# Optimization experiments

Measured on AMD Instinct MI355X. Metric: run time of the kernel, lower is better.

Reference implementation:

```python
import jax, jax.numpy as jnp
import numpy as np


def setup_inputs() -> dict:
    key = jax.random.key(0)
    k1, k2, k3 = jax.random.split(key, 3)
    B, H, S, D = 2, 8, 4096, 64
    queries = jax.random.normal(k1, (B, H, S, D), dtype=jnp.float32)
    keys = jax.random.normal(k2, (B, H, S, D), dtype=jnp.float32)
    values = jax.random.normal(k3, (B, H, S, D), dtype=jnp.float32)
    mask = jnp.zeros((1, 1, S, S), dtype=jnp.float32)
    return {"queries": queries, "keys": keys, "values": values, "d_k": D, "mask": mask}


def reference(queries, keys, values, d_k, mask):
    # scores: [B, H, Sq, Sk]
    scale = 1.0 / jnp.sqrt(jnp.asarray(d_k, dtype=queries.dtype))
    scores = jnp.einsum("bhqd,bhkd->bhqk", queries, keys) * scale
    scores = scores + (-1e9) * mask  # additive mask, broadcasts over B, H
    weights = jax.nn.softmax(scores, axis=-1)
    return jnp.einsum("bhqk,bhkd->bhqd", weights, values)
```

## Files before the change

kernel.cpp:

```cpp
#include <hip/hip_runtime.h>

#define S_LEN 4096
#define DHEAD 64
#define BQ    128
#define BK    64
#define NT    (S_LEN / BK)
#define KPAD  72
#define NBH   16
#define TILE_HALFS (BK * DHEAD)
#define WS_KV_HALFS ((size_t)NBH * NT * TILE_HALFS)

typedef __fp16   pk16x2 __attribute__((ext_vector_type(2)));
typedef _Float16 half4v __attribute__((ext_vector_type(4)));
typedef _Float16 half8  __attribute__((ext_vector_type(8)));
typedef float    f32x4  __attribute__((ext_vector_type(4)));

__device__ __forceinline__ void gl_lds16(const _Float16* g, _Float16* l) {
    __builtin_amdgcn_global_load_lds(
        (const __attribute__((address_space(1))) unsigned int*)g,
        (__attribute__((address_space(3))) unsigned int*)l, 16, 0, 0);
}

__global__ void mask_flag_kernel(const float4* __restrict__ mask, int* __restrict__ flag) {
    const long stride = 2048L * 256;
    long i = (long)blockIdx.x * 256 + threadIdx.x;
    int nz = 0;
    #pragma unroll
    for (int it = 0; it < 8; ++it) {
        float4 a = mask[i + it * stride];
        nz |= (a.x != 0.f) | (a.y != 0.f) | (a.z != 0.f) | (a.w != 0.f);
    }
    if (__any(nz)) {
        if ((threadIdx.x & 63) == 0) atomicOr(flag, 1);
    }
}

__global__ void conv_kernel(const float* __restrict__ Kg, const float* __restrict__ Vg,
                            const float* __restrict__ mask,
                            _Float16* __restrict__ wsK, _Float16* __restrict__ wsV,
                            int* __restrict__ flag) {
    const int tid  = threadIdx.x;
    const int tile = blockIdx.x;
    __shared__ __align__(16) _Float16 T[64][64];

    if (blockIdx.y == 0) {
        const float* Ksrc = Kg + (long)tile * TILE_HALFS;
        _Float16*    dst  = wsK + (long)tile * TILE_HALFS;
        #pragma unroll
        for (int it = 0; it < 2; ++it) {
            int m = tid + it * 256;
            int r = m >> 3, c = m & 7;
            const float4* s4 = (const float4*)(Ksrc + r * DHEAD + ((c ^ (r & 7)) << 3));
            float4 a = s4[0], b = s4[1];
            union { pk16x2 p[4]; half8 h; } u;
            u.p[0] = __builtin_amdgcn_cvt_pkrtz(a.x, a.y);
            u.p[1] = __builtin_amdgcn_cvt_pkrtz(a.z, a.w);
            u.p[2] = __builtin_amdgcn_cvt_pkrtz(b.x, b.y);
            u.p[3] = __builtin_amdgcn_cvt_pkrtz(b.z, b.w);
            *(half8*)(dst + m * 8) = u.h;
        }
    } else if (blockIdx.y == 1) {
        const float* Vsrc = Vg + (long)tile * TILE_HALFS;
        const int r  = tid >> 2;
        const int d0 = (tid & 3) << 4;
        const float4* s4 = (const float4*)(Vsrc + r * DHEAD + d0);
        float vv[16];
        *(float4*)&vv[0]  = s4[0];
        *(float4*)&vv[4]  = s4[1];
        *(float4*)&vv[8]  = s4[2];
        *(float4*)&vv[12] = s4[3];
        #pragma unroll
        for (int j = 0; j < 16; j += 2) {
            pk16x2 p = __builtin_amdgcn_cvt_pkrtz(vv[j], vv[j + 1]);
            T[d0 + j][r]     = *((_Float16*)&p);
            T[d0 + j + 1][r] = *((_Float16*)&p + 1);
        }
        __syncthreads();
        _Float16* dst = wsV + (long)tile * TILE_HALFS;
        #pragma unroll
        for (int it = 0; it < 2; ++it) {
            int m = tid + it * 256;
            int d = m >> 3, c = m & 7;
            *(half8*)(dst + m * 8) = *(const half8*)&T[d][(c ^ (d & 7)) << 3];
        }
    } else {
        const float4* m4 = (const float4*)mask;
        const long stride = 1024L * 256;
        long i = (long)blockIdx.x * 256 + tid;
        int nz = 0;
        #pragma unroll
        for (int it = 0; it < 16; ++it) {
            float4 a = m4[i + it * stride];
            nz |= (a.x != 0.f) | (a.y != 0.f) | (a.z != 0.f) | (a.w != 0.f);
        }
        if (__any(nz)) {
            if ((tid & 63) == 0) atomicOr(flag, 1);
        }
    }
}

__global__ __launch_bounds__(256, 4) void attn_ws_kernel(
    const float* __restrict__ Q, const _Float16* __restrict__ KW,
    const _Float16* __restrict__ VW, const int* __restrict__ dk,
    const float* __restrict__ mask, const int* __restrict__ maskflag,
    float* __restrict__ O)
{
    const int qt   = blockIdx.x;
    const int bh   = blockIdx.y;
    const int tid  = threadIdx.x;
    const int wave = tid >> 6;
    const int lane = tid & 63;
    const int l15  = lane & 15;
    const int quad = lane >> 4;
    const int sw   = (l15 & 7) << 3;
    const int rq8  = quad << 3;

    const long base = (long)bh * S_LEN * DHEAD;
    const float* Qh = Q + base;
    float*       Oh = O + base;
    const _Float16* gk = KW + (long)bh * (NT * TILE_HALFS);
    const _Float16* gv = VW + (long)bh * (NT * TILE_HALFS);

    const int q0 = qt * 64 + wave * 16;
    const float csq  = rsqrtf((float)dk[0]) * 1.44269504088896f;
    const float mfac = -1e9f * 1.44269504088896f;
    const bool use_mask = (maskflag[0] != 0);

    __shared__ __align__(16) _Float16 KT[2][TILE_HALFS];
    __shared__ __align__(16) _Float16 VT[2][TILE_HALFS];
    __shared__ __align__(16) _Float16 Pw[4][16][64];

    half8 qf[2];
    #pragma unroll
    for (int kc = 0; kc < 2; ++kc) {
        const float4* src = (const float4*)(Qh + (long)(q0 + l15) * DHEAD + kc*32 + rq8);
        float4 a = src[0], b = src[1];
        union { pk16x2 p[4]; half8 h; } u;
        u.p[0] = __builtin_amdgcn_cvt_pkrtz(a.x*csq, a.y*csq);
        u.p[1] = __builtin_amdgcn_cvt_pkrtz(a.z*csq, a.w*csq);
        u.p[2] = __builtin_amdgcn_cvt_pkrtz(b.x*csq, b.y*csq);
        u.p[3] = __builtin_amdgcn_cvt_pkrtz(b.z*csq, b.w*csq);
        qf[kc] = u.h;
    }

    auto stage = [&](int kt, int b) {
        const _Float16* k8 = gk + (long)kt * TILE_HALFS + tid * 8;
        const _Float16* v8 = gv + (long)kt * TILE_HALFS + tid * 8;
        gl_lds16(k8,        &KT[b][tid * 8]);
        gl_lds16(k8 + 2048, &KT[b][2048 + tid * 8]);
        gl_lds16(v8,        &VT[b][tid * 8]);
        gl_lds16(v8 + 2048, &VT[b][2048 + tid * 8]);
    };

    f32x4 o[4];
    #pragma unroll
    for (int dt = 0; dt < 4; ++dt) o[dt] = (f32x4){0.f, 0.f, 0.f, 0.f};
    float m_i = -INFINITY;
    float l_i = 0.0f;

    stage(0, 0);
    __syncthreads();

    for (int kt = 0; kt < NT; ++kt) {
        const int b = kt & 1;
        if (kt + 1 < NT) stage(kt + 1, b ^ 1);

        f32x4 st[4];
        #pragma unroll
        for (int nt = 0; nt < 4; ++nt) st[nt] = (f32x4){0.f,0.f,0.f,0.f};
        __builtin_amdgcn_s_setprio(1);
        #pragma unroll
        for (int nt = 0; nt < 4; ++nt) {
            const int rb = (nt << 10) + (l15 << 6);
            #pragma unroll
            for (int kc = 0; kc < 2; ++kc) {
                half8 af = *(const half8*)&KT[b][rb + ((kc*32 + rq8) ^ sw)];
                st[nt] = __builtin_amdgcn_mfma_f32_16x16x32_f16(af, qf[kc], st[nt], 0, 0, 0);
            }
        }
        __builtin_amdgcn_s_setprio(0);

        if (use_mask) {
            const long mrow = (long)(q0 + l15) * S_LEN + kt*BK;
            #pragma unroll
            for (int nt = 0; nt < 4; ++nt)
                #pragma unroll
                for (int r = 0; r < 4; ++r)
                    st[nt][r] += mfac * mask[mrow + nt*16 + quad*4 + r];
        }

        {
            float mx = fmaxf(fmaxf(fmaxf(st[0][0], st[0][1]), fmaxf(st[0][2], st[0][3])),
                             fmaxf(fmaxf(st[1][0], st[1][1]), fmaxf(st[1][2], st[1][3])));
            float mx2 = fmaxf(fmaxf(fmaxf(st[2][0], st[2][1]), fmaxf(st[2][2], st[2][3])),
                              fmaxf(fmaxf(st[3][0], st[3][1]), fmaxf(st[3][2], st[3][3])));
            mx = fmaxf(mx, mx2);
            mx = fmaxf(mx, __shfl_xor(mx, 16, 64));
            mx = fmaxf(mx, __shfl_xor(mx, 32, 64));
            const bool need = __any(mx > m_i);
            const float mnew = need ? fmaxf(m_i, mx) : m_i;
            float rsum = 0.0f;
            #pragma unroll
            for (int nt = 0; nt < 4; ++nt) {
                #pragma unroll
                for (int r = 0; r < 4; ++r) {
                    float p = __builtin_amdgcn_exp2f(st[nt][r] - mnew);
                    st[nt][r] = p;
                    rsum += p;
                }
            }
            rsum += __shfl_xor(rsum, 16, 64);
            rsum += __shfl_xor(rsum, 32, 64);
            if (need) {
                const float alpha = __builtin_amdgcn_exp2f(m_i - mnew);
                #pragma unroll
                for (int r = 0; r < 4; ++r) {
                    float a_r = __shfl(alpha, quad*4 + r, 64);
                    #pragma unroll
                    for (int dt = 0; dt < 4; ++dt) o[dt][r] *= a_r;
                }
                l_i = alpha * l_i + rsum;
                m_i = mnew;
            } else {
                l_i += rsum;
            }
        }

        #pragma unroll
        for (int nt = 0; nt < 4; ++nt) {
            union { pk16x2 p[2]; half4v h; } up;
            up.p[0] = __builtin_amdgcn_cvt_pkrtz(st[nt][0], st[nt][1]);
            up.p[1] = __builtin_amdgcn_cvt_pkrtz(st[nt][2], st[nt][3]);
            *(half4v*)&Pw[wave][l15][(nt*16 + quad*4) ^ sw] = up.h;
        }

        __builtin_amdgcn_s_setprio(1);
        #pragma unroll
        for (int kc2 = 0; kc2 < 2; ++kc2) {
            half8 pa = *(const half8*)&Pw[wave][l15][(kc2*32 + rq8) ^ sw];
            #pragma unroll
            for (int dt = 0; dt < 4; ++dt) {
                const int db = (dt << 10) + (l15 << 6);
                half8 vb = *(const half8*)&VT[b][db + ((kc2*32 + rq8) ^ sw)];
                o[dt] = __builtin_amdgcn_mfma_f32_16x16x32_f16(pa, vb, o[dt], 0, 0, 0);
            }
        }
        __builtin_amdgcn_s_setprio(0);

        if (kt + 1 < NT) __syncthreads();
    }

    #pragma unroll
    for (int r = 0; r < 4; ++r) {
        float lq = __shfl(l_i, quad*4 + r, 64);
        float linv = __builtin_amdgcn_rcpf(lq);
        const long row = (long)(q0 + quad*4 + r) * DHEAD;
        #pragma unroll
        for (int dt = 0; dt < 4; ++dt)
            Oh[row + dt*16 + l15] = o[dt][r] * linv;
    }
}

__global__ __launch_bounds__(256, 2) void attn_kernel_fb(
    const float* __restrict__ Q, const float* __restrict__ K,
    const float* __restrict__ V, const int* __restrict__ dk,
    const float* __restrict__ mask, const int* __restrict__ maskflag,
    float* __restrict__ O)
{
    const int qt   = blockIdx.x;
    const int bh   = blockIdx.y;
    const int tid  = threadIdx.x;
    const int wave = tid >> 6;
    const int lane = tid & 63;
    const int l15  = lane & 15;
    const int quad = lane >> 4;

    const long base = (long)bh * S_LEN * DHEAD;
    const float* Qh = Q + base;
    const float* Kh = K + base;
    const float* Vh = V + base;
    float*       Oh = O + base;

    const int q0 = qt * BQ + wave * 32;
    const float csq  = rsqrtf((float)dk[0]) * 1.44269504088896f;
    const float mfac = -1e9f * 1.44269504088896f;
    const bool use_mask = (maskflag[0] != 0);

    __shared__ __align__(16) _Float16 Kt[2][BK][KPAD];
    __shared__ __align__(16) _Float16 Vt[2][DHEAD * KPAD];
    __shared__ __align__(16) _Float16 Pw[4][32][KPAD];

    half8 qf[2][2];
    #pragma unroll
    for (int f = 0; f < 2; ++f) {
        #pragma unroll
        for (int kc = 0; kc < 2; ++kc) {
            const float4* src = (const float4*)(Qh + (long)(q0 + f*16 + l15) * DHEAD + kc*32 + quad*8);
            float4 a = src[0], b = src[1];
            union { pk16x2 p[4]; half8 h; } u;
            u.p[0] = __builtin_amdgcn_cvt_pkrtz(a.x*csq, a.y*csq);
            u.p[1] = __builtin_amdgcn_cvt_pkrtz(a.z*csq, a.w*csq);
            u.p[2] = __builtin_amdgcn_cvt_pkrtz(b.x*csq, b.y*csq);
            u.p[3] = __builtin_amdgcn_cvt_pkrtz(b.z*csq, b.w*csq);
            qf[f][kc] = u.h;
        }
    }

    const int kr  = tid >> 2;
    const int ks  = tid & 3;
    const int vrp = tid >> 3;
    const int vdq = tid & 7;
    const float* Kb = Kh + (long)kr * DHEAD + ks * 16;
    const float* Vb = Vh + (long)(2 * vrp) * DHEAD + vdq * 8;
    const int vcol = (((vrp >> 2) ^ vdq) << 3) + ((2 * vrp) & 7);
    const int vd0  = vdq * 8;

    float4 kf[4], vf[4];
    auto load_tile = [&](int kt) {
        const float4* kp  = (const float4*)(Kb + (long)kt * BK * DHEAD);
        kf[0] = kp[0]; kf[1] = kp[1]; kf[2] = kp[2]; kf[3] = kp[3];
        const float4* vp0 = (const float4*)(Vb + (long)kt * BK * DHEAD);
        const float4* vp1 = (const float4*)(Vb + (long)kt * BK * DHEAD + DHEAD);
        vf[0] = vp0[0]; vf[1] = vp0[1]; vf[2] = vp1[0]; vf[3] = vp1[1];
    };
    auto store_tile = [&](int b) {
        union { pk16x2 p[4]; half8 h; } u0, u1;
        u0.p[0] = __builtin_amdgcn_cvt_pkrtz(kf[0].x, kf[0].y);
        u0.p[1] = __builtin_amdgcn_cvt_pkrtz(kf[0].z, kf[0].w);
        u0.p[2] = __builtin_amdgcn_cvt_pkrtz(kf[1].x, kf[1].y);
        u0.p[3] = __builtin_amdgcn_cvt_pkrtz(kf[1].z, kf[1].w);
        u1.p[0] = __builtin_amdgcn_cvt_pkrtz(kf[2].x, kf[2].y);
        u1.p[1] = __builtin_amdgcn_cvt_pkrtz(kf[2].z, kf[2].w);
        u1.p[2] = __builtin_amdgcn_cvt_pkrtz(kf[3].x, kf[3].y);
        u1.p[3] = __builtin_amdgcn_cvt_pkrtz(kf[3].z, kf[3].w);
        *(half8*)&Kt[b][kr][ks*16]     = u0.h;
        *(half8*)&Kt[b][kr][ks*16 + 8] = u1.h;
        _Float16* vt = &Vt[b][0];
        *(pk16x2*)&vt[(vd0+0)*KPAD + vcol] = __builtin_amdgcn_cvt_pkrtz(vf[0].x, vf[2].x);
        *(pk16x2*)&vt[(vd0+1)*KPAD + vcol] = __builtin_amdgcn_cvt_pkrtz(vf[0].y, vf[2].y);
        *(pk16x2*)&vt[(vd0+2)*KPAD + vcol] = __builtin_amdgcn_cvt_pkrtz(vf[0].z, vf[2].z);
        *(pk16x2*)&vt[(vd0+3)*KPAD + vcol] = __builtin_amdgcn_cvt_pkrtz(vf[0].w, vf[2].w);
        *(pk16x2*)&vt[(vd0+4)*KPAD + vcol] = __builtin_amdgcn_cvt_pkrtz(vf[1].x, vf[3].x);
        *(pk16x2*)&vt[(vd0+5)*KPAD + vcol] = __builtin_amdgcn_cvt_pkrtz(vf[1].y, vf[3].y);
        *(pk16x2*)&vt[(vd0+6)*KPAD + vcol] = __builtin_amdgcn_cvt_pkrtz(vf[1].z, vf[3].z);
        *(pk16x2*)&vt[(vd0+7)*KPAD + vcol] = __builtin_amdgcn_cvt_pkrtz(vf[1].w, vf[3].w);
    };

    f32x4 o[2][4];
    #pragma unroll
    for (int f = 0; f < 2; ++f)
        #pragma unroll
        for (int dt = 0; dt < 4; ++dt) o[f][dt] = (f32x4){0.f, 0.f, 0.f, 0.f};
    float m_i[2] = {-INFINITY, -INFINITY};
    float l_i[2] = {0.0f, 0.0f};

    load_tile(0);
    store_tile(0);
    __syncthreads();

    for (int kt = 0; kt < NT; ++kt) {
        const int b = kt & 1;
        if (kt + 1 < NT) load_tile(kt + 1);

        f32x4 st[2][4];
        #pragma unroll
        for (int f = 0; f < 2; ++f)
            #pragma unroll
            for (int nt = 0; nt < 4; ++nt) st[f][nt] = (f32x4){0.f,0.f,0.f,0.f};
        #pragma unroll
        for (int nt = 0; nt < 4; ++nt) {
            #pragma unroll
            for (int kc = 0; kc < 2; ++kc) {
                half8 af = *(const half8*)&Kt[b][nt*16 + l15][kc*32 + quad*8];
                st[0][nt] = __builtin_amdgcn_mfma_f32_16x16x32_f16(af, qf[0][kc], st[0][nt], 0, 0, 0);
                st[1][nt] = __builtin_amdgcn_mfma_f32_16x16x32_f16(af, qf[1][kc], st[1][nt], 0, 0, 0);
            }
        }

        if (use_mask) {
            #pragma unroll
            for (int f = 0; f < 2; ++f) {
                const long mrow = (long)(q0 + f*16 + l15) * S_LEN + kt*BK;
                #pragma unroll
                for (int nt = 0; nt < 4; ++nt)
                    #pragma unroll
                    for (int r = 0; r < 4; ++r)
                        st[f][nt][r] += mfac * mask[mrow + nt*16 + quad*4 + r];
            }
        }

        float alpha[2];
        #pragma unroll
        for (int f = 0; f < 2; ++f) {
            float mx = fmaxf(fmaxf(fmaxf(st[f][0][0], st[f][0][1]), fmaxf(st[f][0][2], st[f][0][3])),
                             fmaxf(fmaxf(st[f][1][0], st[f][1][1]), fmaxf(st[f][1][2], st[f][1][3])));
            float mx2 = fmaxf(fmaxf(fmaxf(st[f][2][0], st[f][2][1]), fmaxf(st[f][2][2], st[f][2][3])),
                              fmaxf(fmaxf(st[f][3][0], st[f][3][1]), fmaxf(st[f][3][2], st[f][3][3])));
            mx = fmaxf(mx, mx2);
            mx = fmaxf(mx, __shfl_xor(mx, 16, 64));
            mx = fmaxf(mx, __shfl_xor(mx, 32, 64));
            float mnew = fmaxf(m_i[f], mx);
            float rsum = 0.0f;
            #pragma unroll
            for (int nt = 0; nt < 4; ++nt) {
                #pragma unroll
                for (int r = 0; r < 4; ++r) {
                    float p = __builtin_amdgcn_exp2f(st[f][nt][r] - mnew);
                    st[f][nt][r] = p;
                    rsum += p;
                }
            }
            rsum += __shfl_xor(rsum, 16, 64);
            rsum += __shfl_xor(rsum, 32, 64);
            alpha[f] = __builtin_amdgcn_exp2f(m_i[f] - mnew);
            l_i[f] = alpha[f] * l_i[f] + rsum;
            m_i[f] = mnew;
        }

        #pragma unroll
        for (int f = 0; f < 2; ++f)
            #pragma unroll
            for (int r = 0; r < 4; ++r) {
                float a_r = __shfl(alpha[f], quad*4 + r, 64);
                #pragma unroll
                for (int dt = 0; dt < 4; ++dt) o[f][dt][r] *= a_r;
            }

        #pragma unroll
        for (int f = 0; f < 2; ++f)
            #pragma unroll
            for (int nt = 0; nt < 4; ++nt) {
                union { pk16x2 p[2]; half4v h; } up;
                up.p[0] = __builtin_amdgcn_cvt_pkrtz(st[f][nt][0], st[f][nt][1]);
                up.p[1] = __builtin_amdgcn_cvt_pkrtz(st[f][nt][2], st[f][nt][3]);
                *(half4v*)&Pw[wave][f*16 + l15][nt*16 + quad*4] = up.h;
            }

        #pragma unroll
        for (int kc2 = 0; kc2 < 2; ++kc2) {
            half8 pa0 = *(const half8*)&Pw[wave][l15][kc2*32 + quad*8];
            half8 pa1 = *(const half8*)&Pw[wave][16 + l15][kc2*32 + quad*8];
            #pragma unroll
            for (int dt = 0; dt < 4; ++dt) {
                const int row = dt*16 + l15;
                const int pb  = (4*kc2 + quad) ^ (row >> 3);
                half8 vb = *(const half8*)&Vt[b][row*KPAD + pb*8];
                o[0][dt] = __builtin_amdgcn_mfma_f32_16x16x32_f16(pa0, vb, o[0][dt], 0, 0, 0);
                o[1][dt] = __builtin_amdgcn_mfma_f32_16x16x32_f16(pa1, vb, o[1][dt], 0, 0, 0);
            }
        }

        if (kt + 1 < NT) {
            store_tile((kt + 1) & 1);
            __syncthreads();
        }
    }

    #pragma unroll
    for (int f = 0; f < 2; ++f) {
        #pragma unroll
        for (int r = 0; r < 4; ++r) {
            float lq = __shfl(l_i[f], quad*4 + r, 64);
            float linv = __builtin_amdgcn_rcpf(lq);
            const long row = (long)(q0 + f*16 + quad*4 + r) * DHEAD;
            #pragma unroll
            for (int dt = 0; dt < 4; ++dt)
                Oh[row + dt*16 + l15] = o[f][dt][r] * linv;
        }
    }
}

extern "C" void kernel_launch(void* const* d_in, const int* in_sizes, int n_in,
                              void* d_out, int out_size, void* d_ws, size_t ws_size,
                              hipStream_t stream) {
    const float* Q    = (const float*)d_in[0];
    const float* K    = (const float*)d_in[1];
    const float* V    = (const float*)d_in[2];
    const int*   dk   = (const int*)d_in[3];
    const float* mask = (const float*)d_in[4];
    float* out = (float*)d_out;
    int* flag = (int*)d_ws;

    (void)hipMemsetAsync(flag, 0, sizeof(int), stream);

    const size_t WS_NEED = 256 + 2 * WS_KV_HALFS * sizeof(_Float16);

    if (ws_size >= WS_NEED) {
        _Float16* wsK = (_Float16*)((char*)d_ws + 256);
        _Float16* wsV = wsK + WS_KV_HALFS;
        conv_kernel<<<dim3(NBH * NT, 3), 256, 0, stream>>>(K, V, mask, wsK, wsV, flag);
        dim3 grid(S_LEN / 64, NBH);
        attn_ws_kernel<<<grid, 256, 0, stream>>>(Q, wsK, wsV, dk, mask, flag, out);
    } else {
        mask_flag_kernel<<<2048, 256, 0, stream>>>((const float4*)mask, flag);
        dim3 grid(S_LEN / BQ, NBH);
        attn_kernel_fb<<<grid, 256, 0, stream>>>(Q, K, V, dk, mask, flag, out);
    }
}
```

Measured before the change: 263.7 us.

## Switch attention to 32x32 MFMA tiles with register-resident P and split-K combine

Replaces the 16x16x32 MFMA attention kernel with a 32x32x16 MFMA version that handles 128 queries per block (32 per wave). The P matrix is passed between the two matmuls through permlane32_swap in registers instead of an LDS round trip. It also splits the key range in two, giving 1024 blocks, and adds a combine kernel that merges the partial outputs using the saved max and sum. The block index is remapped across 8 groups, which appears aimed at XCD locality. The goal is more MFMA throughput per instruction, less LDS traffic and better occupancy, at the cost of an extra kernel launch and extra global traffic for the partial outputs.

After: 270.6 us. +2.6%, slower.

```diff
diff --git a/kernel.cpp b/kernel.cpp
--- a/kernel.cpp
+++ b/kernel.cpp
@@ -2,11 +2,11 @@
 
 #define S_LEN 4096
 #define DHEAD 64
-#define BQ    128
 #define BK    64
 #define NT    (S_LEN / BK)
+#define NBH   16
 #define KPAD  72
-#define NBH   16
+#define BQ    128
 #define TILE_HALFS (BK * DHEAD)
 #define WS_KV_HALFS ((size_t)NBH * NT * TILE_HALFS)
 
@@ -14,11 +14,33 @@
 typedef _Float16 half4v __attribute__((ext_vector_type(4)));
 typedef _Float16 half8  __attribute__((ext_vector_type(8)));
 typedef float    f32x4  __attribute__((ext_vector_type(4)));
+typedef float    f32x16 __attribute__((ext_vector_type(16)));
+typedef unsigned uint2v __attribute__((ext_vector_type(2)));
+
+#define MFMA32(a, b, c) __builtin_amdgcn_mfma_f32_32x32x16_f16(a, b, c, 0, 0, 0)
 
 __device__ __forceinline__ void gl_lds16(const _Float16* g, _Float16* l) {
     __builtin_amdgcn_global_load_lds(
         (const __attribute__((address_space(1))) unsigned int*)g,
         (__attribute__((address_space(3))) unsigned int*)l, 16, 0, 0);
+}
+
+__device__ __forceinline__ unsigned pk2u(float a, float b) {
+    union { pk16x2 p; unsigned u; } x;
+    x.p = __builtin_amdgcn_cvt_pkrtz(a, b);
+    return x.u;
+}
+
+__device__ __forceinline__ uint2v pls(unsigned x, unsigned y) {
+    return __builtin_amdgcn_permlane32_swap(x, y, false, false);
+}
+__device__ __forceinline__ float xmax32(float v) {
+    uint2v r = pls(__float_as_uint(v), __float_as_uint(v));
+    return fmaxf(__uint_as_float(r.x), __uint_as_float(r.y));
+}
+__device__ __forceinline__ float xadd32(float v) {
+    uint2v r = pls(__float_as_uint(v), __float_as_uint(v));
+    return __uint_as_float(r.x) + __uint_as_float(r.y);
 }
 
 __global__ void mask_flag_kernel(const float4* __restrict__ mask, int* __restrict__ flag) {
@@ -99,125 +121,130 @@
     }
 }
 
-__global__ __launch_bounds__(256, 4) void attn_ws_kernel(
+template <int SPLIT>
+__global__ __launch_bounds__(256, 4) void attn32_kernel(
     const float* __restrict__ Q, const _Float16* __restrict__ KW,
-    const _Float16* __restrict__ VW, const int* __restrict__ dk,
+    const _Float16* __restrict__ VW, const int* __restrict__ dkp,
     const float* __restrict__ mask, const int* __restrict__ maskflag,
-    float* __restrict__ O)
+    float* __restrict__ O1, float* __restrict__ O2, float* __restrict__ ML)
 {
-    const int qt   = blockIdx.x;
-    const int bh   = blockIdx.y;
+    const int fid = blockIdx.x;
+    int bh, half, qt;
+    if (SPLIT == 2) {
+        const int L = (fid & 7) * 128 + (fid >> 3);
+        bh = L >> 6; half = (L >> 5) & 1; qt = L & 31;
+    } else {
+        const int L = (fid & 7) * 64 + (fid >> 3);
+        bh = L >> 5; half = 0; qt = L & 31;
+    }
+    const int HT  = NT / SPLIT;
+    const int kt0 = half * HT;
+
     const int tid  = threadIdx.x;
     const int wave = tid >> 6;
     const int lane = tid & 63;
-    const int l15  = lane & 15;
-    const int quad = lane >> 4;
-    const int sw   = (l15 & 7) << 3;
-    const int rq8  = quad << 3;
+    const int l31  = lane & 31;
+    const int h    = lane >> 5;
+    const int cx   = lane & 7;
+    const bool hib = (lane >= 32);
 
     const long base = (long)bh * S_LEN * DHEAD;
     const float* Qh = Q + base;
-    float*       Oh = O + base;
     const _Float16* gk = KW + (long)bh * (NT * TILE_HALFS);
     const _Float16* gv = VW + (long)bh * (NT * TILE_HALFS);
 
-    const int q0 = qt * 64 + wave * 16;
-    const float csq  = rsqrtf((float)dk[0]) * 1.44269504088896f;
+    const int q0 = qt * 128 + wave * 32;
+    const float csq  = rsqrtf((float)dkp[0]) * 1.44269504088896f;
     const float mfac = -1e9f * 1.44269504088896f;
     const bool use_mask = (maskflag[0] != 0);
 
     __shared__ __align__(16) _Float16 KT[2][TILE_HALFS];
     __shared__ __align__(16) _Float16 VT[2][TILE_HALFS];
-    __shared__ __align__(16) _Float16 Pw[4][16][64];
-
-    half8 qf[2];
+
+    half8 qf[4];
     #pragma unroll
-    for (int kc = 0; kc < 2; ++kc) {
-        const float4* src = (const float4*)(Qh + (long)(q0 + l15) * DHEAD + kc*32 + rq8);
+    for (int ks = 0; ks < 4; ++ks) {
+        const float4* src = (const float4*)(Qh + (long)(q0 + l31) * DHEAD + ks * 16 + h * 8);
         float4 a = src[0], b = src[1];
-        union { pk16x2 p[4]; half8 h; } u;
-        u.p[0] = __builtin_amdgcn_cvt_pkrtz(a.x*csq, a.y*csq);
-        u.p[1] = __builtin_amdgcn_cvt_pkrtz(a.z*csq, a.w*csq);
-        u.p[2] = __builtin_amdgcn_cvt_pkrtz(b.x*csq, b.y*csq);
-        u.p[3] = __builtin_amdgcn_cvt_pkrtz(b.z*csq, b.w*csq);
-        qf[kc] = u.h;
-    }
-
-    auto stage = [&](int kt, int b) {
+        union { unsigned u[4]; half8 h8; } u;
+        u.u[0] = pk2u(a.x * csq, a.y * csq);
+        u.u[1] = pk2u(a.z * csq, a.w * csq);
+        u.u[2] = pk2u(b.x * csq, b.y * csq);
+        u.u[3] = pk2u(b.z * csq, b.w * csq);
+        qf[ks] = u.h8;
+    }
+
+    auto stage = [&](int kt, int bb) {
         const _Float16* k8 = gk + (long)kt * TILE_HALFS + tid * 8;
         const _Float16* v8 = gv + (long)kt * TILE_HALFS + tid * 8;
-        gl_lds16(k8,        &KT[b][tid * 8]);
-        gl_lds16(k8 + 2048, &KT[b][2048 + tid * 8]);
-        gl_lds16(v8,        &VT[b][tid * 8]);
-        gl_lds16(v8 + 2048, &VT[b][2048 + tid * 8]);
+        gl_lds16(k8,        &KT[bb][tid * 8]);
+        gl_lds16(k8 + 2048, &KT[bb][2048 + tid * 8]);
+        gl_lds16(v8,        &VT[bb][tid * 8]);
+        gl_lds16(v8 + 2048, &VT[bb][2048 + tid * 8]);
     };
 
-    f32x4 o[4];
-    #pragma unroll
-    for (int dt = 0; dt < 4; ++dt) o[dt] = (f32x4){0.f, 0.f, 0.f, 0.f};
+    f32x16 o0 = {0.f,0.f,0.f,0.f,0.f,0.f,0.f,0.f,0.f,0.f,0.f,0.f,0.f,0.f,0.f,0.f};
+    f32x16 o1 = o0;
     float m_i = -INFINITY;
     float l_i = 0.0f;
 
-    stage(0, 0);
+    stage(kt0, 0);
     __syncthreads();
 
-    for (int kt = 0; kt < NT; ++kt) {
-        const int b = kt & 1;
-        if (kt + 1 < NT) stage(kt + 1, b ^ 1);
-
-        f32x4 st[4];
-        #pragma unroll
-        for (int nt = 0; nt < 4; ++nt) st[nt] = (f32x4){0.f,0.f,0.f,0.f};
+    for (int lt = 0; lt < HT; ++lt) {
+        const int kt = kt0 + lt;
+        const int b  = lt & 1;
+        if (lt + 1 < HT) stage(kt + 1, b ^ 1);
+
+        f32x16 s0 = {0.f,0.f,0.f,0.f,0.f,0.f,0.f,0.f,0.f,0.f,0.f,0.f,0.f,0.f,0.f,0.f};
+        f32x16 s1 = s0;
         __builtin_amdgcn_s_setprio(1);
         #pragma unroll
-        for (int nt = 0; nt < 4; ++nt) {
-            const int rb = (nt << 10) + (l15 << 6);
-            #pragma unroll
-            for (int kc = 0; kc < 2; ++kc) {
-                half8 af = *(const half8*)&KT[b][rb + ((kc*32 + rq8) ^ sw)];
-                st[nt] = __builtin_amdgcn_mfma_f32_16x16x32_f16(af, qf[kc], st[nt], 0, 0, 0);
-            }
+        for (int ks = 0; ks < 4; ++ks) {
+            const int off = (((2 * ks + h) ^ cx) << 3);
+            half8 a0 = *(const half8*)&KT[b][(l31 << 6) + off];
+            half8 a1 = *(const half8*)&KT[b][2048 + (l31 << 6) + off];
+            s0 = MFMA32(a0, qf[ks], s0);
+            s1 = MFMA32(a1, qf[ks], s1);
         }
         __builtin_amdgcn_s_setprio(0);
 
         if (use_mask) {
-            const long mrow = (long)(q0 + l15) * S_LEN + kt*BK;
-            #pragma unroll
-            for (int nt = 0; nt < 4; ++nt)
-                #pragma unroll
-                for (int r = 0; r < 4; ++r)
-                    st[nt][r] += mfac * mask[mrow + nt*16 + quad*4 + r];
+            const float* mrow = mask + (long)(q0 + l31) * S_LEN + kt * BK;
+            #pragma unroll
+            for (int r = 0; r < 16; ++r) {
+                const int k = (r & 3) + ((r >> 2) << 3) + (h << 2);
+                s0[r] += mfac * mrow[k];
+                s1[r] += mfac * mrow[32 + k];
+            }
         }
 
         {
-            float mx = fmaxf(fmaxf(fmaxf(st[0][0], st[0][1]), fmaxf(st[0][2], st[0][3])),
-                             fmaxf(fmaxf(st[1][0], st[1][1]), fmaxf(st[1][2], st[1][3])));
-            float mx2 = fmaxf(fmaxf(fmaxf(st[2][0], st[2][1]), fmaxf(st[2][2], st[2][3])),
-                              fmaxf(fmaxf(st[3][0], st[3][1]), fmaxf(st[3][2], st[3][3])));
-            mx = fmaxf(mx, mx2);
-            mx = fmaxf(mx, __shfl_xor(mx, 16, 64));
-            mx = fmaxf(mx, __shfl_xor(mx, 32, 64));
+            float t[8];
+            #pragma unroll
+            for (int i = 0; i < 8; ++i)
+                t[i] = fmaxf(fmaxf(s0[2*i], s0[2*i+1]), fmaxf(s1[2*i], s1[2*i+1]));
+            float mx = fmaxf(fmaxf(fmaxf(t[0], t[1]), fmaxf(t[2], t[3])),
+                             fmaxf(fmaxf(t[4], t[5]), fmaxf(t[6], t[7])));
+            mx = xmax32(mx);
             const bool need = __any(mx > m_i);
             const float mnew = need ? fmaxf(m_i, mx) : m_i;
-            float rsum = 0.0f;
-            #pragma unroll
-            for (int nt = 0; nt < 4; ++nt) {
-                #pragma unroll
-                for (int r = 0; r < 4; ++r) {
-                    float p = __builtin_amdgcn_exp2f(st[nt][r] - mnew);
-                    st[nt][r] = p;
-                    rsum += p;
-                }
-            }
-            rsum += __shfl_xor(rsum, 16, 64);
-            rsum += __shfl_xor(rsum, 32, 64);
+            float ra = 0.f, rb = 0.f;
+            #pragma unroll
+            for (int r = 0; r < 16; ++r) {
+                float p0 = __builtin_amdgcn_exp2f(s0[r] - mnew);
+                float p1 = __builtin_amdgcn_exp2f(s1[r] - mnew);
+                s0[r] = p0; s1[r] = p1;
+                ra += p0; rb += p1;
+            }
+            float rsum = xadd32(ra + rb);
             if (need) {
                 const float alpha = __builtin_amdgcn_exp2f(m_i - mnew);
                 #pragma unroll
-                for (int r = 0; r < 4; ++r) {
-                    float a_r = __shfl(alpha, quad*4 + r, 64);
-                    #pragma unroll
-                    for (int dt = 0; dt < 4; ++dt) o[dt][r] *= a_r;
+                for (int r = 0; r < 16; ++r) {
+                    const int qr = (r & 3) + ((r >> 2) << 3) + (h << 2);
+                    float a_r = __shfl(alpha, qr, 64);
+                    o0[r] *= a_r; o1[r] *= a_r;
                 }
                 l_i = alpha * l_i + rsum;
                 m_i = mnew;
@@ -226,39 +253,85 @@
             }
         }
 
-        #pragma unroll
-        for (int nt = 0; nt < 4; ++nt) {
-            union { pk16x2 p[2]; half4v h; } up;
-            up.p[0] = __builtin_amdgcn_cvt_pkrtz(st[nt][0], st[nt][1]);
-            up.p[1] = __builtin_amdgcn_cvt_pkrtz(st[nt][2], st[nt][3]);
-            *(half4v*)&Pw[wave][l15][(nt*16 + quad*4) ^ sw] = up.h;
+        unsigned plo[16], phi[16];
+        #pragma unroll
+        for (int d = 0; d < 8; ++d) {
+            uint2v r0 = pls(pk2u(s0[2*d], s0[2*d+1]), pk2u(s0[2*d], s0[2*d+1]));
+            plo[d] = r0.x; phi[d] = r0.y;
+            uint2v r1 = pls(pk2u(s1[2*d], s1[2*d+1]), pk2u(s1[2*d], s1[2*d+1]));
+            plo[8 + d] = r1.x; phi[8 + d] = r1.y;
         }
 
         __builtin_amdgcn_s_setprio(1);
         #pragma unroll
-        for (int kc2 = 0; kc2 < 2; ++kc2) {
-            half8 pa = *(const half8*)&Pw[wave][l15][(kc2*32 + rq8) ^ sw];
-            #pragma unroll
-            for (int dt = 0; dt < 4; ++dt) {
-                const int db = (dt << 10) + (l15 << 6);
-                half8 vb = *(const half8*)&VT[b][db + ((kc2*32 + rq8) ^ sw)];
-                o[dt] = __builtin_amdgcn_mfma_f32_16x16x32_f16(pa, vb, o[dt], 0, 0, 0);
-            }
+        for (int s = 0; s < 4; ++s) {
+            const int kb = s >> 1, tq = s & 1, bs = kb * 8 + 4 * tq;
+            union { unsigned u[4]; half8 h8; } pa;
+            pa.u[0] = hib ? plo[bs + 2] : plo[bs + 0];
+            pa.u[1] = hib ? plo[bs + 3] : plo[bs + 1];
+            pa.u[2] = hib ? phi[bs + 2] : phi[bs + 0];
+            pa.u[3] = hib ? phi[bs + 3] : phi[bs + 1];
+            const int off = (((2 * s + h) ^ cx) << 3);
+            half8 v0 = *(const half8*)&VT[b][(l31 << 6) + off];
+            half8 v1 = *(const half8*)&VT[b][2048 + (l31 << 6) + off];
+            o0 = MFMA32(pa.h8, v0, o0);
+            o1 = MFMA32(pa.h8, v1, o1);
         }
         __builtin_amdgcn_s_setprio(0);
 
-        if (kt + 1 < NT) __syncthreads();
-    }
-
-    #pragma unroll
-    for (int r = 0; r < 4; ++r) {
-        float lq = __shfl(l_i, quad*4 + r, 64);
-        float linv = __builtin_amdgcn_rcpf(lq);
-        const long row = (long)(q0 + quad*4 + r) * DHEAD;
-        #pragma unroll
-        for (int dt = 0; dt < 4; ++dt)
-            Oh[row + dt*16 + l15] = o[dt][r] * linv;
-    }
+        if (lt + 1 < HT) __syncthreads();
+    }
+
+    if (SPLIT == 2) {
+        float* dst = ((half == 0) ? O1 : O2) + base;
+        #pragma unroll
+        for (int r = 0; r < 16; ++r) {
+            const int qr = (r & 3) + ((r >> 2) << 3) + (h << 2);
+            const long row = (long)(q0 + qr) * DHEAD;
+            dst[row + l31]      = o0[r];
+            dst[row + 32 + l31] = o1[r];
+        }
+        if (!hib) {
+            float2* ml = (float2*)ML + (long)(half * NBH + bh) * S_LEN + q0 + l31;
+            *ml = make_float2(m_i, l_i);
+        }
+    } else {
+        float* dst = O1 + base;
+        #pragma unroll
+        for (int r = 0; r < 16; ++r) {
+            const int qr = (r & 3) + ((r >> 2) << 3) + (h << 2);
+            float lq = __shfl(l_i, qr, 64);
+            float inv = __builtin_amdgcn_rcpf(lq);
+            const long row = (long)(q0 + qr) * DHEAD;
+            dst[row + l31]      = o0[r] * inv;
+            dst[row + 32 + l31] = o1[r] * inv;
+        }
+    }
+}
+
+__global__ __launch_bounds__(256) void combine_kernel(
+    float* __restrict__ O1, const float* __restrict__ O2,
+    const float* __restrict__ ML)
+{
+    const long flat = (long)blockIdx.x * 256 + threadIdx.x;
+    const int  dg = (int)(flat & 15);
+    const long q  = (flat >> 4) & (S_LEN - 1);
+    const int  bh = (int)(flat >> 16);
+    const float2 ml1 = ((const float2*)ML)[(long)(0 * NBH + bh) * S_LEN + q];
+    const float2 ml2 = ((const float2*)ML)[(long)(1 * NBH + bh) * S_LEN + q];
+    const float m  = fmaxf(ml1.x, ml2.x);
+    const float a1 = __builtin_amdgcn_exp2f(ml1.x - m);
+    const float a2 = __builtin_amdgcn_exp2f(ml2.x - m);
+    const float inv = __builtin_amdgcn_rcpf(ml1.y * a1 + ml2.y * a2);
+    const long idx = ((long)bh * S_LEN + q) * DHEAD + dg * 4;
+    float4 x1 = *(const float4*)&O1[idx];
+    float4 x2 = *(const float4*)&O2[idx];
+    float4 r;
+    r.x = (x1.x * a1 + x2.x * a2) * inv;
+    r.y = (x1.y * a1 + x2.y * a2) * inv;
+    r.z = (x1.z * a1 + x2.z * a2) * inv;
+    r.w = (x1.w * a1 + x2.w * a2) * inv;
+    *(float4*)&O1[idx] = r;
 }
 
 __global__ __launch_bounds__(256, 2) void attn_kernel_fb(
@@ -483,14 +556,24 @@
 
     (void)hipMemsetAsync(flag, 0, sizeof(int), stream);
 
-    const size_t WS_NEED = 256 + 2 * WS_KV_HALFS * sizeof(_Float16);
-
-    if (ws_size >= WS_NEED) {
+    const size_t KV_BYTES = 2 * WS_KV_HALFS * sizeof(_Float16);
+    const size_t O2_BYTES = (size_t)NBH * S_LEN * DHEAD * sizeof(float);
+    const size_t ML_BYTES = 2ull * NBH * S_LEN * 2 * sizeof(float);
+    const size_t NEED_BASE  = 256 + KV_BYTES;
+    const size_t NEED_SPLIT = NEED_BASE + O2_BYTES + ML_BYTES;
+
+    if (ws_size >= NEED_BASE) {
         _Float16* wsK = (_Float16*)((char*)d_ws + 256);
         _Float16* wsV = wsK + WS_KV_HALFS;
         conv_kernel<<<dim3(NBH * NT, 3), 256, 0, stream>>>(K, V, mask, wsK, wsV, flag);
-        dim3 grid(S_LEN / 64, NBH);
-        attn_ws_kernel<<<grid, 256, 0, stream>>>(Q, wsK, wsV, dk, mask, flag, out);
+        if (ws_size >= NEED_SPLIT) {
+            float* O2 = (float*)((char*)d_ws + 256 + KV_BYTES);
+            float* ML = (float*)((char*)d_ws + 256 + KV_BYTES + O2_BYTES);
+            attn32_kernel<2><<<1024, 256, 0, stream>>>(Q, wsK, wsV, dk, mask, flag, out, O2, ML);
+            combine_kernel<<<4096, 256, 0, stream>>>(out, O2, ML);
+        } else {
+            attn32_kernel<1><<<512, 256, 0, stream>>>(Q, wsK, wsV, dk, mask, flag, out, nullptr, nullptr);
+        }
     } else {
         mask_flag_kernel<<<2048, 256, 0, stream>>>((const float4*)mask, flag);
         dim3 grid(S_LEN / BQ, NBH);
```
